# Performance work log

Measured on AMD Instinct MI355X. Metric: run time of the kernel, lower is better.

Reference implementation:

```python
import jax, jax.numpy as jnp
import numpy as np

B, N, K, D, H, FF, L, NH = 8, 50, 20, 3, 128, 2048, 3, 8
S = N * K
HD = H // NH


def setup_inputs() -> dict:
    key = jax.random.key(0)
    ks = jax.random.split(key, 16)
    visited = jax.random.uniform(ks[0], (B, S)) < 0.05
    # the single most-recent action per batch row (status flips 0 -> 1)
    action_idx = jax.random.randint(ks[1], (B,), 0, S)
    visited = visited.at[jnp.arange(B), action_idx].set(True)
    feats = jax.random.normal(ks[2], (B, S, D - 1)) * visited[:, :, None]
    state = jnp.concatenate([feats, visited[:, :, None].astype(jnp.float32)], axis=-1)
    prev_state = state.at[jnp.arange(B), action_idx, :].set(0.0)

    def w(k, shape, s=0.02):
        return jax.random.normal(k, shape, dtype=jnp.float32) * s

    return dict(
        prev_state=prev_state, state=state,
        W_pre=w(ks[3], (D, H)), b_pre=jnp.zeros(H),
        Wq=w(ks[4], (L, H, H)), bq=jnp.zeros((L, H)),
        Wk=w(ks[5], (L, H, H)), bk=jnp.zeros((L, H)),
        Wv=w(ks[6], (L, H, H)), bv=jnp.zeros((L, H)),
        Wo=w(ks[7], (L, H, H)), bo=jnp.zeros((L, H)),
        ln1_g=jnp.ones((L, H)), ln1_b=jnp.zeros((L, H)),
        Wff1=w(ks[8], (L, H, FF)), bff1=jnp.zeros((L, FF)),
        Wff2=w(ks[9], (L, FF, H)), bff2=jnp.zeros((L, H)),
        ln2_g=jnp.ones((L, H)), ln2_b=jnp.zeros((L, H)),
        W_comb=w(ks[10], (2 * H, H)), b_comb=jnp.zeros(H),
        W_dec=w(ks[11], (H, H)), b_dec=jnp.zeros(H),
        W_lin=w(ks[12], (S, S)), b_lin=jnp.zeros(S),
    )


def _layer_norm(x, g, b, eps=1e-5):
    m = jnp.mean(x, -1, keepdims=True)
    v = jnp.mean(jnp.square(x - m), -1, keepdims=True)
    return (x - m) * jax.lax.rsqrt(v + eps) * g + b


def _update_mask(state):
    # vectorized equivalent of the original Python-loop scatter mask
    status = state[:, :, -1] != 0                      # visited [B, S], S = K*N channel-major
    mask = status
    vis_kn = status.reshape(B, K, N)
    user_any = vis_kn.any(axis=1)                      # [B, N]: user visited on any channel
    mask = mask | jnp.broadcast_to(user_any[:, None, :], (B, K, N)).reshape(B, S)
    assigned = state.reshape(B, K, N, D).sum(-1) != 0  # [B, K, N]
    full = assigned.sum(-1) >= 2                       # [B, K]: channel already has 2 users
    mask = mask | jnp.broadcast_to(full[:, :, None], (B, K, N)).reshape(B, S)
    return mask


def reference(prev_state, state, W_pre, b_pre, Wq, bq, Wk, bk, Wv, bv, Wo, bo,
              ln1_g, ln1_b, Wff1, bff1, Wff2, bff2, ln2_g, ln2_b,
              W_comb, b_comb, W_dec, b_dec, W_lin, b_lin):
    mask = _update_mask(state)
    # exactly one status change per batch row (sequential RL step)
    diff = prev_state[:, :, -1] != state[:, :, -1]
    act_idx = jnp.argmax(diff, axis=1)                 # [B]

    x = state @ W_pre + b_pre                          # [B, S, H]
    scale = np.float32(1.0 / np.sqrt(HD))
    for i in range(L):  # 3 post-LN transformer encoder layers
        q = (x @ Wq[i] + bq[i]).reshape(B, S, NH, HD)
        k = (x @ Wk[i] + bk[i]).reshape(B, S, NH, HD)
        v = (x @ Wv[i] + bv[i]).reshape(B, S, NH, HD)
        att = jax.nn.softmax(jnp.einsum('bqhd,bkhd->bhqk', q, k) * scale, axis=-1)
        o = jnp.einsum('bhqk,bkhd->bqhd', att, v).reshape(B, S, H) @ Wo[i] + bo[i]
        x = _layer_norm(x + o, ln1_g[i], ln1_b[i])
        ff = jax.nn.relu(x @ Wff1[i] + bff1[i]) @ Wff2[i] + bff2[i]
        x = _layer_norm(x + ff, ln2_g[i], ln2_b[i])

    last = x[jnp.arange(B), act_idx]                   # [B, H]
    combined = jnp.concatenate([x.mean(axis=1), last], axis=-1)  # [B, 2H]
    g = combined @ W_comb + b_comb                     # [B, H]
    dec = x @ W_dec + b_dec                            # [B, S, H]
    scores = jnp.einsum('bsh,bh->bs', dec, g)          # [B, S]
    masked = scores @ W_lin + b_lin                    # Q-Learning head
    return jnp.where(mask, -jnp.inf, masked)
```

## Files before the change

kernel.cpp:

```cpp
#include <hip/hip_runtime.h>
#include <math.h>

#define Bb 8
#define Ss 1000
#define Kk 20
#define Nn 50
#define Dd 3
#define Hh 128
#define FFf 2048
#define Ll 3
#define NHh 8
#define HDd 16
#define ROWS (Bb*Ss)

#define SENTINEL -3.0e38f

typedef unsigned short ush;
typedef short short8 __attribute__((ext_vector_type(8)));
typedef short short4v __attribute__((ext_vector_type(4)));
typedef float f32x4 __attribute__((ext_vector_type(4)));

__device__ __forceinline__ ush f2b(float f) {
  unsigned x = __float_as_uint(f);
  return (ush)((x + 0x7fff + ((x >> 16) & 1)) >> 16);
}

__global__ __launch_bounds__(256) void mask_kernel(const float* __restrict__ state,
                                                   const float* __restrict__ prev_state,
                                                   int* __restrict__ mask, int* __restrict__ act_idx) {
  int b = blockIdx.x, tid = threadIdx.x;
  __shared__ unsigned char status[Ss], assigned[Ss], uany[Nn], fullk[Kk];
  __shared__ int act;
  if (tid == 0) act = 1 << 30;
  __syncthreads();
  for (int s = tid; s < Ss; s += 256) {
    const float* st = state + ((size_t)b * Ss + s) * Dd;
    float f2 = st[2];
    status[s] = (f2 != 0.f);
    assigned[s] = ((st[0] + st[1] + f2) != 0.f);
    float p2 = prev_state[((size_t)b * Ss + s) * Dd + 2];
    if (p2 != f2) atomicMin(&act, s);
  }
  __syncthreads();
  if (tid < Nn) {
    unsigned char a = 0;
    for (int k = 0; k < Kk; ++k) a |= status[k * Nn + tid];
    uany[tid] = a;
  } else if (tid >= 64 && tid < 64 + Kk) {
    int k = tid - 64, cnt = 0;
    for (int n = 0; n < Nn; ++n) cnt += assigned[k * Nn + n];
    fullk[k] = (cnt >= 2);
  }
  __syncthreads();
  for (int s = tid; s < Ss; s += 256)
    mask[b * Ss + s] = (int)(status[s] | uany[s % Nn] | fullk[s / Nn]);
  if (tid == 0) act_idx[b] = (act >= Ss) ? 0 : act;
}

__global__ __launch_bounds__(256) void pre_kernel(const float* __restrict__ state,
                                                  const float* __restrict__ W_pre,
                                                  const float* __restrict__ b_pre,
                                                  float* __restrict__ x, ush* __restrict__ xbf,
                                                  float* __restrict__ mpart) {
  int idx = blockIdx.x * 256 + threadIdx.x;
  if (idx >= ROWS * Hh) return;
  if (idx < Bb * Hh) mpart[idx] = 0.f;
  int row = idx >> 7, n = idx & 127;
  const float* st = state + (size_t)row * Dd;
  float v = b_pre[n] + st[0] * W_pre[n] + st[1] * W_pre[Hh + n] + st[2] * W_pre[2 * Hh + n];
  x[idx] = v;
  xbf[idx] = f2b(v);
}

#define TQKV 144
#define TWO  48
#define TFF1 768
#define TFF2 768
#define TWD  16
#define TBIAS 5
#define TTOT (TQKV+TWO+TFF1+TFF2+TWD+TBIAS)
__global__ __launch_bounds__(256) void transpose_prep(
    const float* __restrict__ Wq, const float* __restrict__ Wk, const float* __restrict__ Wv,
    const float* __restrict__ Wo, const float* __restrict__ Wff1, const float* __restrict__ Wff2,
    const float* __restrict__ bq, const float* __restrict__ bk, const float* __restrict__ bv,
    const float* __restrict__ W_dec,
    ush* __restrict__ wqkvT, ush* __restrict__ woT, ush* __restrict__ wff1T, ush* __restrict__ wff2T,
    float* __restrict__ bqkv, float* __restrict__ wdecT) {
  int t = blockIdx.x, tid = threadIdx.x;
  if (t >= TTOT - TBIAS) {
    int idx = (t - (TTOT - TBIAS)) * 256 + tid;
    if (idx < Ll * 384) {
      int l = idx / 384, c = idx % 384;
      bqkv[idx] = (c < 128) ? bq[l * Hh + c] : (c < 256 ? bk[l * Hh + c - 128] : bv[l * Hh + c - 256]);
    }
    return;
  }
  __shared__ float lf[32][33];
  int tr = tid >> 5, tc = tid & 31;
  const float* s; ush* d = nullptr; float* df = nullptr;
  int sp, dp;
  if (t < TQKV) {
    int l = t / 48, rem = t % 48, mat = rem / 16, tt = rem % 16;
    int ti = tt >> 2, tj = tt & 3;
    const float* m = (mat == 0) ? Wq : (mat == 1) ? Wk : Wv;
    s = m + (size_t)l * 16384 + (size_t)(ti * 32) * 128 + tj * 32; sp = 128;
    d = wqkvT + ((size_t)l * 384 + mat * 128 + tj * 32) * 128 + ti * 32; dp = 128;
  } else if (t < TQKV + TWO) {
    int r0 = t - TQKV; int l = r0 / 16, tt = r0 % 16, ti = tt >> 2, tj = tt & 3;
    s = Wo + (size_t)l * 16384 + (size_t)(ti * 32) * 128 + tj * 32; sp = 128;
    d = woT + ((size_t)l * 128 + tj * 32) * 128 + ti * 32; dp = 128;
  } else if (t < TQKV + TWO + TFF1) {
    int r0 = t - TQKV - TWO; int l = r0 / 256, tt = r0 % 256, ti = tt >> 6, tj = tt & 63;
    s = Wff1 + (size_t)l * 128 * 2048 + (size_t)(ti * 32) * 2048 + tj * 32; sp = 2048;
    d = wff1T + ((size_t)l * 2048 + tj * 32) * 128 + ti * 32; dp = 128;
  } else if (t < TQKV + TWO + TFF1 + TFF2) {
    int r0 = t - TQKV - TWO - TFF1; int l = r0 / 256, tt = r0 % 256, ti = tt >> 2, tj = tt & 3;
    s = Wff2 + (size_t)l * 2048 * 128 + (size_t)(ti * 32) * 128 + tj * 32; sp = 128;
    d = wff2T + ((size_t)l * 128 + tj * 32) * 2048 + ti * 32; dp = 2048;
  } else {
    int tt = t - TQKV - TWO - TFF1 - TFF2; int ti = tt >> 2, tj = tt & 3;
    s = W_dec + (size_t)(ti * 32) * 128 + tj * 32; sp = 128;
    df = wdecT + (size_t)(tj * 32) * 128 + ti * 32; dp = 128;
  }
#pragma unroll
  for (int p = 0; p < 4; ++p) {
    int r = tr + p * 8;
    lf[r][tc] = s[(size_t)r * sp + tc];
  }
  __syncthreads();
#pragma unroll
  for (int p = 0; p < 4; ++p) {
    int r = tr + p * 8;
    if (d) d[(size_t)r * dp + tc] = f2b(lf[tc][r]);
    else   df[(size_t)r * dp + tc] = lf[tc][r];
  }
}

#define LDP 40
template <int RELU, int QKVV>
__global__ __launch_bounds__(256) void gemm_mfma(const ush* __restrict__ A, const ush* __restrict__ Wt,
                                                 const float* __restrict__ bias, ush* __restrict__ out,
                                                 int N, int K, ush* __restrict__ vTout) {
  __shared__ ush As[2][64 * LDP];
  __shared__ ush Bs[2][64 * LDP];
  int tid = threadIdx.x;
  int lane = tid & 63, wid = tid >> 6;
  int wr = wid >> 1, wc = wid & 1;
  int m0 = blockIdx.y * 64, n0 = blockIdx.x * 64;
  int lrow = tid >> 2, lk = (tid & 3) << 3;
  int quad = lane >> 4, l16 = lane & 15, kb = quad << 3;

  const ush* Ap = A + (size_t)(m0 + lrow) * K + lk;
  const ush* Bp = Wt + (size_t)(n0 + lrow) * K + lk;

  f32x4 acc[2][2];
#pragma unroll
  for (int i = 0; i < 2; ++i)
#pragma unroll
    for (int j = 0; j < 2; ++j) acc[i][j] = (f32x4){0.f, 0.f, 0.f, 0.f};

  short8 pa = *(const short8*)Ap;
  short8 pb = *(const short8*)Bp;
  *(short8*)&As[0][lrow * LDP + lk] = pa;
  *(short8*)&Bs[0][lrow * LDP + lk] = pb;
  __syncthreads();

  int NT = K >> 5;
  for (int it = 0; it < NT; ++it) {
    int cur = it & 1;
    bool have = (it + 1 < NT);
    if (have) {
      pa = *(const short8*)(Ap + (it + 1) * 32);
      pb = *(const short8*)(Bp + (it + 1) * 32);
    }
    short8 a0 = *(short8*)&As[cur][(wr * 32 + l16) * LDP + kb];
    short8 a1 = *(short8*)&As[cur][(wr * 32 + 16 + l16) * LDP + kb];
    short8 b0 = *(short8*)&Bs[cur][(wc * 32 + l16) * LDP + kb];
    short8 b1 = *(short8*)&Bs[cur][(wc * 32 + 16 + l16) * LDP + kb];
    acc[0][0] = __builtin_amdgcn_mfma_f32_16x16x32_bf16(a0, b0, acc[0][0], 0, 0, 0);
    acc[0][1] = __builtin_amdgcn_mfma_f32_16x16x32_bf16(a0, b1, acc[0][1], 0, 0, 0);
    acc[1][0] = __builtin_amdgcn_mfma_f32_16x16x32_bf16(a1, b0, acc[1][0], 0, 0, 0);
    acc[1][1] = __builtin_amdgcn_mfma_f32_16x16x32_bf16(a1, b1, acc[1][1], 0, 0, 0);
    if (have) {
      *(short8*)&As[cur ^ 1][lrow * LDP + lk] = pa;
      *(short8*)&Bs[cur ^ 1][lrow * LDP + lk] = pb;
    }
    __syncthreads();
  }

#pragma unroll
  for (int i = 0; i < 2; ++i)
#pragma unroll
    for (int j = 0; j < 2; ++j) {
      int col = n0 + wc * 32 + j * 16 + l16;
      int rbase = m0 + wr * 32 + i * 16 + quad * 4;
      float bval = bias[col];
      if (QKVV && col >= 256) {
        int bb2 = rbase / 1000, qq = rbase - bb2 * 1000;
        short4v pk;
#pragma unroll
        for (int v = 0; v < 4; ++v) pk[v] = (short)f2b(acc[i][j][v] + bval);
        *(short4v*)&vTout[((size_t)(bb2 * 128 + (col - 256))) * 1024 + qq] = pk;
      } else {
#pragma unroll
        for (int v = 0; v < 4; ++v) {
          float o = acc[i][j][v] + bval;
          if (RELU) o = fmaxf(o, 0.f);
          out[(size_t)(rbase + v) * N + col] = f2b(o);
        }
      }
    }
}

#define F2P 72
template <int MEANOUT>
__global__ __launch_bounds__(512) void gemm_ln_kernel(const ush* __restrict__ A,
                                                      const ush* __restrict__ Wt,
                                                      const float* __restrict__ bias,
                                                      const float* __restrict__ ln_g, const float* __restrict__ ln_b,
                                                      float* __restrict__ x, ush* __restrict__ xbf,
                                                      float* __restrict__ mpart) {
  const int KK = 2048;
  __shared__ ush As[2][32 * F2P];
  __shared__ ush Bs[2][128 * F2P];
  __shared__ float red1[2][4][16], red2[2][4][16];
  __shared__ float pbias[128], pg[128], pb[128];

  int tid = threadIdx.x, lane = tid & 63, w = tid >> 6;
  int wr = w & 1, wc = w >> 1;
  int l16 = lane & 15, quad = lane >> 4, kb = quad * 8;
  int m0 = blockIdx.x * 32;
  if (tid < 128) { pbias[tid] = bias[tid]; pg[tid] = ln_g[tid]; pb[tid] = ln_b[tid]; }

  f32x4 acc[2];
  acc[0] = (f32x4){0.f, 0.f, 0.f, 0.f};
  acc[1] = (f32x4){0.f, 0.f, 0.f, 0.f};

  int arow = tid >> 3, alk = (tid & 7) << 3;
  int brow = tid >> 2, bc = (tid & 3) << 4;
  const ush* Ap = A + (size_t)(m0 + arow) * KK + alk;
  const ush* Bp = Wt + (size_t)brow * KK + bc;

  short8 ra_a, rb_a, ra_b0, ra_b1, rb_b0, rb_b1;

  if (tid < 256) ra_a = *(const short8*)Ap;
  ra_b0 = *(const short8*)Bp;
  ra_b1 = *(const short8*)(Bp + 8);
  if (tid < 256) *(short8*)&As[0][arow * F2P + alk] = ra_a;
  *(short8*)&Bs[0][brow * F2P + bc] = ra_b0;
  *(short8*)&Bs[0][brow * F2P + bc + 8] = ra_b1;
  if (tid < 256) rb_a = *(const short8*)(Ap + 64);
  rb_b0 = *(const short8*)(Bp + 64);
  rb_b1 = *(const short8*)(Bp + 64 + 8);
  __syncthreads();

  for (int k = 0; k < 16; ++k) {
    int t2 = 2 * k + 2, t3 = 2 * k + 3;
    if (t2 < 32) {
      if (tid < 256) ra_a = *(const short8*)(Ap + t2 * 64);
      ra_b0 = *(const short8*)(Bp + t2 * 64);
      ra_b1 = *(const short8*)(Bp + t2 * 64 + 8);
    }
#pragma unroll
    for (int kk = 0; kk < 2; ++kk) {
      short8 a = *(short8*)&As[0][(wr * 16 + l16) * F2P + kk * 32 + kb];
#pragma unroll
      for (int j = 0; j < 2; ++j) {
        short8 b = *(short8*)&Bs[0][(wc * 32 + j * 16 + l16) * F2P + kk * 32 + kb];
        acc[j] = __builtin_amdgcn_mfma_f32_16x16x32_bf16(a, b, acc[j], 0, 0, 0);
      }
    }
    if (tid < 256) *(short8*)&As[1][arow * F2P + alk] = rb_a;
    *(short8*)&Bs[1][brow * F2P + bc] = rb_b0;
    *(short8*)&Bs[1][brow * F2P + bc + 8] = rb_b1;
    __syncthreads();
    if (t3 < 32) {
      if (tid < 256) rb_a = *(const short8*)(Ap + t3 * 64);
      rb_b0 = *(const short8*)(Bp + t3 * 64);
      rb_b1 = *(const short8*)(Bp + t3 * 64 + 8);
    }
#pragma unroll
    for (int kk = 0; kk < 2; ++kk) {
      short8 a = *(short8*)&As[1][(wr * 16 + l16) * F2P + kk * 32 + kb];
#pragma unroll
      for (int j = 0; j < 2; ++j) {
        short8 b = *(short8*)&Bs[1][(wc * 32 + j * 16 + l16) * F2P + kk * 32 + kb];
        acc[j] = __builtin_amdgcn_mfma_f32_16x16x32_bf16(a, b, acc[j], 0, 0, 0);
      }
    }
    if (t2 < 32) {
      if (tid < 256) *(short8*)&As[0][arow * F2P + alk] = ra_a;
      *(short8*)&Bs[0][brow * F2P + bc] = ra_b0;
      *(short8*)&Bs[0][brow * F2P + bc + 8] = ra_b1;
    }
    __syncthreads();
  }

  float v[2][4], s1[4] = {0.f, 0.f, 0.f, 0.f}, s2[4] = {0.f, 0.f, 0.f, 0.f};
#pragma unroll
  for (int j = 0; j < 2; ++j) {
    int col = wc * 32 + j * 16 + l16;
#pragma unroll
    for (int r = 0; r < 4; ++r) {
      int row = m0 + wr * 16 + quad * 4 + r;
      float vv = acc[j][r] + pbias[col] + x[(size_t)row * Hh + col];
      v[j][r] = vv; s1[r] += vv; s2[r] += vv * vv;
    }
  }
#pragma unroll
  for (int m = 1; m <= 8; m <<= 1) {
#pragma unroll
    for (int r = 0; r < 4; ++r) { s1[r] += __shfl_xor(s1[r], m); s2[r] += __shfl_xor(s2[r], m); }
  }
  if (l16 == 0) {
#pragma unroll
    for (int r = 0; r < 4; ++r) {
      red1[wr][wc][quad * 4 + r] = s1[r];
      red2[wr][wc][quad * 4 + r] = s2[r];
    }
  }
  __syncthreads();
  float osum[2] = {0.f, 0.f};
#pragma unroll
  for (int r = 0; r < 4; ++r) {
    int qr = quad * 4 + r;
    float t1 = red1[wr][0][qr] + red1[wr][1][qr] + red1[wr][2][qr] + red1[wr][3][qr];
    float t2 = red2[wr][0][qr] + red2[wr][1][qr] + red2[wr][2][qr] + red2[wr][3][qr];
    float mean = t1 * (1.f / 128.f);
    float var = t2 * (1.f / 128.f) - mean * mean;
    float rstd = rsqrtf(var + 1e-5f);
    int row = m0 + wr * 16 + qr;
#pragma unroll
    for (int j = 0; j < 2; ++j) {
      int col = wc * 32 + j * 16 + l16;
      float o = (v[j][r] - mean) * rstd * pg[col] + pb[col];
      size_t gi = (size_t)row * Hh + col;
      x[gi] = o; xbf[gi] = f2b(o);
      if (MEANOUT) osum[j] += o;
    }
  }
  if (MEANOUT) {
    int gb = (m0 + wr * 16 + quad * 4) / 1000;
#pragma unroll
    for (int j = 0; j < 2; ++j)
      atomicAdd(&mpart[gb * 128 + wc * 32 + j * 16 + l16], osum[j]);
  }
}

__global__ __launch_bounds__(256) void gemm_ln16(const ush* __restrict__ A,
                                                 const ush* __restrict__ Wt,
                                                 const float* __restrict__ bias,
                                                 const float* __restrict__ ln_g, const float* __restrict__ ln_b,
                                                 float* __restrict__ x, ush* __restrict__ xbf) {
  __shared__ ush As[2][16 * F2P];
  __shared__ ush Bs[2][128 * F2P];
  __shared__ float red1[4][16], red2[4][16];
  __shared__ float pbias[128], pg[128], pb[128];

  int tid = threadIdx.x, lane = tid & 63, w = tid >> 6;
  int l16 = lane & 15, quad = lane >> 4, kb = quad * 8;
  int m0 = blockIdx.x * 16;
  if (tid < 128) { pbias[tid] = bias[tid]; pg[tid] = ln_g[tid]; pb[tid] = ln_b[tid]; }

  f32x4 acc[2];
  acc[0] = (f32x4){0.f, 0.f, 0.f, 0.f};
  acc[1] = (f32x4){0.f, 0.f, 0.f, 0.f};

  int srow = tid >> 3, slk = (tid & 7) << 3;
  const ush* Ap = A + (size_t)(m0 + srow) * 128 + slk;
  const ush* Bp = Wt + (size_t)srow * 128 + slk;

  short8 pa;
  short8 pbr[4];
  if (tid < 128) pa = *(const short8*)Ap;
#pragma unroll
  for (int rep = 0; rep < 4; ++rep)
    pbr[rep] = *(const short8*)(Bp + (size_t)rep * 32 * 128);
  if (tid < 128) *(short8*)&As[0][srow * F2P + slk] = pa;
#pragma unroll
  for (int rep = 0; rep < 4; ++rep)
    *(short8*)&Bs[0][(rep * 32 + srow) * F2P + slk] = pbr[rep];
  __syncthreads();

#pragma unroll
  for (int it = 0; it < 2; ++it) {
    if (it == 0) {
      if (tid < 128) pa = *(const short8*)(Ap + 64);
#pragma unroll
      for (int rep = 0; rep < 4; ++rep)
        pbr[rep] = *(const short8*)(Bp + (size_t)rep * 32 * 128 + 64);
    }
#pragma unroll
    for (int kk = 0; kk < 2; ++kk) {
      short8 a = *(short8*)&As[it][l16 * F2P + kk * 32 + kb];
#pragma unroll
      for (int j = 0; j < 2; ++j) {
        short8 b = *(short8*)&Bs[it][(w * 32 + j * 16 + l16) * F2P + kk * 32 + kb];
        acc[j] = __builtin_amdgcn_mfma_f32_16x16x32_bf16(a, b, acc[j], 0, 0, 0);
      }
    }
    if (it == 0) {
      if (tid < 128) *(short8*)&As[1][srow * F2P + slk] = pa;
#pragma unroll
      for (int rep = 0; rep < 4; ++rep)
        *(short8*)&Bs[1][(rep * 32 + srow) * F2P + slk] = pbr[rep];
    }
    __syncthreads();
  }

  float v[2][4], s1[4] = {0.f, 0.f, 0.f, 0.f}, s2[4] = {0.f, 0.f, 0.f, 0.f};
#pragma unroll
  for (int j = 0; j < 2; ++j) {
    int col = w * 32 + j * 16 + l16;
#pragma unroll
    for (int r = 0; r < 4; ++r) {
      int row = m0 + quad * 4 + r;
      float vv = acc[j][r] + pbias[col] + x[(size_t)row * Hh + col];
      v[j][r] = vv; s1[r] += vv; s2[r] += vv * vv;
    }
  }
#pragma unroll
  for (int m = 1; m <= 8; m <<= 1) {
#pragma unroll
    for (int r = 0; r < 4; ++r) { s1[r] += __shfl_xor(s1[r], m); s2[r] += __shfl_xor(s2[r], m); }
  }
  if (l16 == 0) {
#pragma unroll
    for (int r = 0; r < 4; ++r) {
      red1[w][quad * 4 + r] = s1[r];
      red2[w][quad * 4 + r] = s2[r];
    }
  }
  __syncthreads();
#pragma unroll
  for (int r = 0; r < 4; ++r) {
    int qr = quad * 4 + r;
    float t1 = red1[0][qr] + red1[1][qr] + red1[2][qr] + red1[3][qr];
    float t2 = red2[0][qr] + red2[1][qr] + red2[2][qr] + red2[3][qr];
    float mean = t1 * (1.f / 128.f);
    float var = t2 * (1.f / 128.f) - mean * mean;
    float rstd = rsqrtf(var + 1e-5f);
    int row = m0 + qr;
#pragma unroll
    for (int j = 0; j < 2; ++j) {
      int col = w * 32 + j * 16 + l16;
      float o = (v[j][r] - mean) * rstd * pg[col] + pb[col];
      size_t gi = (size_t)row * Hh + col;
      x[gi] = o; xbf[gi] = f2b(o);
    }
  }
}

__global__ __launch_bounds__(256) void attn_mfma(const ush* __restrict__ qkv,
                                                 const ush* __restrict__ vT,
                                                 ush* __restrict__ attn_o) {
  int blk = blockIdx.x;
  int local = blk >> 3;
  int bh = ((blk & 7) << 3) | (local >> 4);
  int qt = local & 15;
  int b = bh >> 3, h = bh & 7;
  int qbase = qt * 64;
  int tid = threadIdx.x, lane = tid & 63, w = tid >> 6;
  int l16 = lane & 15, quad = lane >> 4, kb = quad * 8;

  __shared__ ush Ks[2][64][40];
  __shared__ ush Vs[2][16][72];
  __shared__ ush Pb[4][16][72];

  if (tid < 128) {
    int row = tid >> 1, g = tid & 1;
    *(short8*)&Ks[0][row][16 + g * 8] = (short8){0, 0, 0, 0, 0, 0, 0, 0};
    *(short8*)&Ks[1][row][16 + g * 8] = (short8){0, 0, 0, 0, 0, 0, 0, 0};
  }

  int qrow = qbase + w * 16 + l16; if (qrow >= Ss) qrow = Ss - 1;
  short8 aq = *(const short8*)(qkv + (size_t)(b * Ss + qrow) * 384 + h * HDd + kb);

  int srow = tid >> 1, sg = tid & 1;
  int sd = (tid - 128) >> 3, skg = (tid - 128) & 7;
  const ush* kbase = qkv + (size_t)b * Ss * 384 + 128 + h * HDd;
  const ush* vbase = vT + (size_t)(b * 128 + h * 16) * 1024;

  if (tid < 128) {
    short8 s8 = (short8){0, 0, 0, 0, 0, 0, 0, 0};
    if (srow < Ss) s8 = *(const short8*)(kbase + (size_t)srow * 384 + sg * 8);
    *(short8*)&Ks[0][srow][sg * 8] = s8;
  } else {
    *(short8*)&Vs[0][sd][skg * 8] = *(const short8*)(vbase + (size_t)sd * 1024 + skg * 8);
  }
  __syncthreads();

  const short one_b = (short)0x3F80;
  const short8 ones = (short8){one_b, one_b, one_b, one_b, one_b, one_b, one_b, one_b};
  f32x4 acc_pv = (f32x4){0.f, 0.f, 0.f, 0.f};
  f32x4 acc_l = (f32x4){0.f, 0.f, 0.f, 0.f};
  const f32x4 zero4 = (f32x4){0.f, 0.f, 0.f, 0.f};

  for (int it = 0; it < 16; ++it) {
    int k0 = it * 64;
    int cur = it & 1, nxt = cur ^ 1;
    bool have = (it + 1 < 16);

    short8 gk, gv;
    if (have) {
      if (tid < 128) {
        gk = (short8){0, 0, 0, 0, 0, 0, 0, 0};
        int key = k0 + 64 + srow;
        if (key < Ss) gk = *(const short8*)(kbase + (size_t)key * 384 + sg * 8);
      } else {
        gv = *(const short8*)(vbase + (size_t)sd * 1024 + k0 + 64 + skg * 8);
      }
    }

    bool tail = (k0 + 64 > Ss);
#pragma unroll
    for (int kn = 0; kn < 4; ++kn) {
      short8 ak = *(short8*)&Ks[cur][kn * 16 + l16][kb];
      f32x4 s = __builtin_amdgcn_mfma_f32_16x16x32_bf16(ak, aq, zero4, 0, 0, 0);
      float p0 = __expf(s[0] * 0.25f);
      float p1 = __expf(s[1] * 0.25f);
      float p2 = __expf(s[2] * 0.25f);
      float p3 = __expf(s[3] * 0.25f);
      if (tail) {
        int keyb = k0 + kn * 16 + quad * 4;
        if (keyb + 0 >= Ss) p0 = 0.f;
        if (keyb + 1 >= Ss) p1 = 0.f;
        if (keyb + 2 >= Ss) p2 = 0.f;
        if (keyb + 3 >= Ss) p3 = 0.f;
      }
      unsigned lo, hi;
      asm("v_cvt_pk_bf16_f32 %0, %1, %2" : "=v"(lo) : "v"(p0), "v"(p1));
      asm("v_cvt_pk_bf16_f32 %0, %1, %2" : "=v"(hi) : "v"(p2), "v"(p3));
      *(uint2*)&Pb[w][l16][kn * 16 + quad * 4] = make_uint2(lo, hi);
    }

    short8 pa0 = *(short8*)&Pb[w][l16][kb];
    short8 pa1 = *(short8*)&Pb[w][l16][32 + kb];
    short8 vb0 = *(short8*)&Vs[cur][l16][kb];
    short8 vb1 = *(short8*)&Vs[cur][l16][32 + kb];
    acc_pv = __builtin_amdgcn_mfma_f32_16x16x32_bf16(pa0, vb0, acc_pv, 0, 0, 0);
    acc_pv = __builtin_amdgcn_mfma_f32_16x16x32_bf16(pa1, vb1, acc_pv, 0, 0, 0);
    acc_l = __builtin_amdgcn_mfma_f32_16x16x32_bf16(pa0, ones, acc_l, 0, 0, 0);
    acc_l = __builtin_amdgcn_mfma_f32_16x16x32_bf16(pa1, ones, acc_l, 0, 0, 0);

    if (have) {
      if (tid < 128) *(short8*)&Ks[nxt][srow][sg * 8] = gk;
      else *(short8*)&Vs[nxt][sd][skg * 8] = gv;
    }
    __syncthreads();
  }

#pragma unroll
  for (int r = 0; r < 4; ++r) {
    int q = qbase + w * 16 + quad * 4 + r;
    if (q < Ss)
      attn_o[((size_t)(b * Ss + q)) * Hh + h * HDd + l16] = f2b(acc_pv[r] / acc_l[r]);
  }
}

__global__ __launch_bounds__(128) void ghc_kernel(const float* __restrict__ x, const float* __restrict__ mpart,
                                                  const int* __restrict__ act_idx,
                                                  const float* __restrict__ W_comb, const float* __restrict__ b_comb,
                                                  const float* __restrict__ wdecT, const float* __restrict__ b_dec,
                                                  float* __restrict__ h, float* __restrict__ cb) {
  int b = blockIdx.x, n = threadIdx.x;
  __shared__ float cs[2 * Hh], gs[Hh], red[2];
  cs[n] = mpart[b * Hh + n] * (1.f / Ss);
  cs[Hh + n] = x[((size_t)b * Ss + act_idx[b]) * Hh + n];
  __syncthreads();
  float acc = b_comb[n];
  for (int j = 0; j < 2 * Hh; ++j) acc += cs[j] * W_comb[(size_t)j * Hh + n];
  gs[n] = acc;
  __syncthreads();
  float hv = 0.f;
  for (int c = 0; c < Hh; ++c) hv += wdecT[(size_t)c * Hh + n] * gs[c];
  h[b * Hh + n] = hv;
  float t = b_dec[n] * gs[n];
  for (int off = 32; off; off >>= 1) t += __shfl_down(t, off);
  if ((n & 63) == 0) red[n >> 6] = t;
  __syncthreads();
  if (n == 0) cb[b] = red[0] + red[1];
}

__global__ __launch_bounds__(256) void scores_kernel(const float* __restrict__ x, const float* __restrict__ h,
                                                     const float* __restrict__ cb, float* __restrict__ scores) {
  int wid = threadIdx.x >> 6, lane = threadIdx.x & 63;
  int row = blockIdx.x * 4 + wid;
  if (row >= ROWS) return;
  int b = row / Ss;
  const float* xr = x + (size_t)row * Hh;
  const float* hb = h + b * Hh;
  float s = xr[lane] * hb[lane] + xr[lane + 64] * hb[lane + 64];
  for (int off = 32; off; off >>= 1) s += __shfl_down(s, off);
  if (lane == 0) scores[row] = s + cb[b];
}

__global__ __launch_bounds__(256) void final_part(const float* __restrict__ scores,
                                                  const float* __restrict__ W_lin,
                                                  float* __restrict__ fpart) {
  int spc = blockIdx.x, kc = blockIdx.y;
  int tid = threadIdx.x;
  __shared__ float ss[8][125];
  for (int i = tid; i < 8 * 125; i += 256) {
    int bb = i / 125, s = i - bb * 125;
    ss[bb][s] = scores[bb * Ss + kc * 125 + s];
  }
  __syncthreads();
  if (tid < 250) {
    int sp = spc * 250 + tid;
    float acc[8];
#pragma unroll
    for (int bb = 0; bb < 8; ++bb) acc[bb] = 0.f;
    const float* wl = &W_lin[(size_t)(kc * 125) * Ss + sp];
#pragma unroll 5
    for (int s = 0; s < 125; ++s) {
      float wv = wl[(size_t)s * Ss];
#pragma unroll
      for (int bb = 0; bb < 8; ++bb) acc[bb] = fmaf(ss[bb][s], wv, acc[bb]);
    }
#pragma unroll
    for (int bb = 0; bb < 8; ++bb)
      fpart[((size_t)kc * Bb + bb) * Ss + sp] = acc[bb];
  }
}

__global__ __launch_bounds__(256) void final_combine(const float* __restrict__ fpart,
                                                     const float* __restrict__ b_lin,
                                                     const int* __restrict__ mask,
                                                     float* __restrict__ out) {
  int b = blockIdx.y;
  int sp = blockIdx.x * 256 + threadIdx.x;
  if (sp >= Ss) return;
  float acc = b_lin[sp];
#pragma unroll
  for (int kc = 0; kc < 8; ++kc) acc += fpart[((size_t)kc * Bb + b) * Ss + sp];
  out[b * Ss + sp] = mask[b * Ss + sp] ? SENTINEL : acc;
}

extern "C" void kernel_launch(void* const* d_in, const int* in_sizes, int n_in,
                              void* d_out, int out_size, void* d_ws, size_t ws_size,
                              hipStream_t stream) {
  const float* prev_state = (const float*)d_in[0];
  const float* state = (const float*)d_in[1];
  const float* W_pre = (const float*)d_in[2];
  const float* b_pre = (const float*)d_in[3];
  const float* Wq = (const float*)d_in[4];
  const float* bq = (const float*)d_in[5];
  const float* Wk = (const float*)d_in[6];
  const float* bk = (const float*)d_in[7];
  const float* Wv = (const float*)d_in[8];
  const float* bv = (const float*)d_in[9];
  const float* Wo = (const float*)d_in[10];
  const float* bo = (const float*)d_in[11];
  const float* ln1_g = (const float*)d_in[12];
  const float* ln1_b = (const float*)d_in[13];
  const float* Wff1 = (const float*)d_in[14];
  const float* bff1 = (const float*)d_in[15];
  const float* Wff2 = (const float*)d_in[16];
  const float* bff2 = (const float*)d_in[17];
  const float* ln2_g = (const float*)d_in[18];
  const float* ln2_b = (const float*)d_in[19];
  const float* W_comb = (const float*)d_in[20];
  const float* b_comb = (const float*)d_in[21];
  const float* W_dec = (const float*)d_in[22];
  const float* b_dec = (const float*)d_in[23];
  const float* W_lin = (const float*)d_in[24];
  const float* b_lin = (const float*)d_in[25];

  char* wsp = (char*)d_ws;
  auto alloc = [&](size_t bytes) { char* p = wsp; wsp += (bytes + 255) & ~(size_t)255; return p; };
  int* mask = (int*)alloc(ROWS * 4);
  int* act = (int*)alloc(Bb * 4);
  ush* wqkvT = (ush*)alloc((size_t)Ll * 384 * 128 * 2);
  ush* woT = (ush*)alloc((size_t)Ll * 128 * 128 * 2);
  ush* wff1T = (ush*)alloc((size_t)Ll * 2048 * 128 * 2);
  ush* wff2T = (ush*)alloc((size_t)Ll * 128 * 2048 * 2);
  float* bqkv = (float*)alloc((size_t)Ll * 384 * 4);
  float* wdecT = (float*)alloc((size_t)Hh * Hh * 4);
  float* x = (float*)alloc((size_t)ROWS * Hh * 4);
  ush* xbf = (ush*)alloc((size_t)ROWS * Hh * 2);
  ush* qkv_bf = (ush*)alloc((size_t)ROWS * 384 * 2);
  ush* vT = (ush*)alloc((size_t)Bb * 128 * 1024 * 2);
  ush* attn_ob = (ush*)alloc((size_t)ROWS * Hh * 2);
  float* mpart = (float*)alloc((size_t)Bb * Hh * 4);
  float* hbuf = (float*)alloc((size_t)Bb * Hh * 4);
  float* cb = (float*)alloc((size_t)Bb * 4);
  float* scores = (float*)alloc((size_t)ROWS * 4);
  float* fpart = (float*)alloc((size_t)8 * Bb * Ss * 4);
  ush* ffb = (ush*)alloc((size_t)ROWS * FFf * 2);

  transpose_prep<<<dim3(TTOT), 256, 0, stream>>>(Wq, Wk, Wv, Wo, Wff1, Wff2, bq, bk, bv, W_dec,
                                                 wqkvT, woT, wff1T, wff2T, bqkv, wdecT);
  mask_kernel<<<Bb, 256, 0, stream>>>(state, prev_state, mask, act);
  pre_kernel<<<dim3((ROWS * Hh + 255) / 256), 256, 0, stream>>>(state, W_pre, b_pre, x, xbf, mpart);

  for (int l = 0; l < Ll; ++l) {
    gemm_mfma<0, 1><<<dim3(384 / 64, ROWS / 64), 256, 0, stream>>>(
        xbf, wqkvT + (size_t)l * 384 * 128, bqkv + l * 384, qkv_bf, 384, 128, vT);
    attn_mfma<<<dim3(1024), 256, 0, stream>>>(qkv_bf, vT, attn_ob);
    gemm_ln16<<<dim3(ROWS / 16), 256, 0, stream>>>(
        attn_ob, woT + (size_t)l * 128 * 128, bo + l * Hh, ln1_g + l * Hh, ln1_b + l * Hh, x, xbf);
    gemm_mfma<1, 0><<<dim3(2048 / 64, ROWS / 64), 256, 0, stream>>>(
        xbf, wff1T + (size_t)l * 2048 * 128, bff1 + l * FFf, ffb, 2048, 128, nullptr);
    if (l == Ll - 1)
      gemm_ln_kernel<1><<<dim3(ROWS / 32), 512, 0, stream>>>(
          ffb, wff2T + (size_t)l * 128 * 2048, bff2 + l * Hh, ln2_g + l * Hh, ln2_b + l * Hh, x, xbf, mpart);
    else
      gemm_ln_kernel<0><<<dim3(ROWS / 32), 512, 0, stream>>>(
          ffb, wff2T + (size_t)l * 128 * 2048, bff2 + l * Hh, ln2_g + l * Hh, ln2_b + l * Hh, x, xbf, mpart);
  }

  ghc_kernel<<<Bb, 128, 0, stream>>>(x, mpart, act, W_comb, b_comb, wdecT, b_dec, hbuf, cb);
  scores_kernel<<<dim3(ROWS / 4), 256, 0, stream>>>(x, hbuf, cb, scores);
  final_part<<<dim3(4, 8), 256, 0, stream>>>(scores, W_lin, fpart);
  final_combine<<<dim3(4, Bb), 256, 0, stream>>>(fpart, b_lin, mask, (float*)d_out);
}
```

Measured before the change: 363.6 us.

## Fuse FF1 and FF2 GEMMs with LayerNorm, keeping the hidden activations in LDS

Replaces the separate FF1 GEMM and the FF2+LayerNorm kernel with one kernel. For each block of 32 rows it computes 64-wide chunks of the ReLU hidden layer into shared memory and feeds them straight into the FF2 accumulation, with double-buffered W1/W2 tiles. This removes the write and re-read of the 8000x2048 bf16 intermediate buffer in every layer, plus one kernel launch per layer. In exchange there are more barriers per chunk, and every block streams the full W1 and W2 weights through L2.

Result: no change. 357.0 us, median of 2 (-1.8%).

```diff
diff --git a/kernel.cpp b/kernel.cpp
--- a/kernel.cpp
+++ b/kernel.cpp
@@ -212,86 +212,139 @@
     }
 }
 
-#define F2P 72
+#define XP 136
+#define WP 72
 template <int MEANOUT>
-__global__ __launch_bounds__(512) void gemm_ln_kernel(const ush* __restrict__ A,
-                                                      const ush* __restrict__ Wt,
-                                                      const float* __restrict__ bias,
-                                                      const float* __restrict__ ln_g, const float* __restrict__ ln_b,
-                                                      float* __restrict__ x, ush* __restrict__ xbf,
-                                                      float* __restrict__ mpart) {
-  const int KK = 2048;
-  __shared__ ush As[2][32 * F2P];
-  __shared__ ush Bs[2][128 * F2P];
+__global__ __launch_bounds__(512) void ff_fused(const ush* __restrict__ xin,
+                                                const ush* __restrict__ w1T,
+                                                const ush* __restrict__ w2T,
+                                                const float* __restrict__ b1,
+                                                const float* __restrict__ bias,
+                                                const float* __restrict__ ln_g, const float* __restrict__ ln_b,
+                                                float* __restrict__ x, ush* __restrict__ xbf,
+                                                float* __restrict__ mpart) {
+  __shared__ ush xs[32][XP];
+  __shared__ ush W1L[2][64][XP];
+  __shared__ ush W2L[2][128][WP];
+  __shared__ ush hs[32][WP];
+  __shared__ float pbias[128], pg[128], pb[128];
   __shared__ float red1[2][4][16], red2[2][4][16];
-  __shared__ float pbias[128], pg[128], pb[128];
 
   int tid = threadIdx.x, lane = tid & 63, w = tid >> 6;
-  int wr = w & 1, wc = w >> 1;
+  int f = w & 3, xr = w >> 2;
   int l16 = lane & 15, quad = lane >> 4, kb = quad * 8;
   int m0 = blockIdx.x * 32;
+
+  { int row = tid >> 4, seg = (tid & 15) << 3;
+    *(short8*)&xs[row][seg] = *(const short8*)(xin + (size_t)(m0 + row) * 128 + seg); }
   if (tid < 128) { pbias[tid] = bias[tid]; pg[tid] = ln_g[tid]; pb[tid] = ln_b[tid]; }
+
+  int w1row = tid >> 3, w1seg = (tid & 7) << 3;
+  int w2row = tid >> 2, w2seg = (tid & 3) << 4;
+
+  short8 r0a, r0b, r0c, r0d, r1a, r1b, r1c, r1d;
+
+  r0a = *(const short8*)(w1T + (size_t)w1row * 128 + w1seg);
+  r0b = *(const short8*)(w1T + (size_t)w1row * 128 + w1seg + 64);
+  r0c = *(const short8*)(w2T + (size_t)w2row * 2048 + w2seg);
+  r0d = *(const short8*)(w2T + (size_t)w2row * 2048 + w2seg + 8);
+  *(short8*)&W1L[0][w1row][w1seg] = r0a;
+  *(short8*)&W1L[0][w1row][w1seg + 64] = r0b;
+  *(short8*)&W2L[0][w2row][w2seg] = r0c;
+  *(short8*)&W2L[0][w2row][w2seg + 8] = r0d;
+  r1a = *(const short8*)(w1T + (size_t)(64 + w1row) * 128 + w1seg);
+  r1b = *(const short8*)(w1T + (size_t)(64 + w1row) * 128 + w1seg + 64);
+  r1c = *(const short8*)(w2T + (size_t)w2row * 2048 + 64 + w2seg);
+  r1d = *(const short8*)(w2T + (size_t)w2row * 2048 + 64 + w2seg + 8);
+  __syncthreads();
 
   f32x4 acc[2];
   acc[0] = (f32x4){0.f, 0.f, 0.f, 0.f};
   acc[1] = (f32x4){0.f, 0.f, 0.f, 0.f};
-
-  int arow = tid >> 3, alk = (tid & 7) << 3;
-  int brow = tid >> 2, bc = (tid & 3) << 4;
-  const ush* Ap = A + (size_t)(m0 + arow) * KK + alk;
-  const ush* Bp = Wt + (size_t)brow * KK + bc;
-
-  short8 ra_a, rb_a, ra_b0, ra_b1, rb_b0, rb_b1;
-
-  if (tid < 256) ra_a = *(const short8*)Ap;
-  ra_b0 = *(const short8*)Bp;
-  ra_b1 = *(const short8*)(Bp + 8);
-  if (tid < 256) *(short8*)&As[0][arow * F2P + alk] = ra_a;
-  *(short8*)&Bs[0][brow * F2P + bc] = ra_b0;
-  *(short8*)&Bs[0][brow * F2P + bc + 8] = ra_b1;
-  if (tid < 256) rb_a = *(const short8*)(Ap + 64);
-  rb_b0 = *(const short8*)(Bp + 64);
-  rb_b1 = *(const short8*)(Bp + 64 + 8);
-  __syncthreads();
+  const f32x4 zero4 = (f32x4){0.f, 0.f, 0.f, 0.f};
 
   for (int k = 0; k < 16; ++k) {
-    int t2 = 2 * k + 2, t3 = 2 * k + 3;
-    if (t2 < 32) {
-      if (tid < 256) ra_a = *(const short8*)(Ap + t2 * 64);
-      ra_b0 = *(const short8*)(Bp + t2 * 64);
-      ra_b1 = *(const short8*)(Bp + t2 * 64 + 8);
-    }
-#pragma unroll
-    for (int kk = 0; kk < 2; ++kk) {
-      short8 a = *(short8*)&As[0][(wr * 16 + l16) * F2P + kk * 32 + kb];
+    int c0 = 2 * k, c1 = 2 * k + 1;
+    if (c0 + 2 < 32) {
+      r0a = *(const short8*)(w1T + (size_t)((c0 + 2) * 64 + w1row) * 128 + w1seg);
+      r0b = *(const short8*)(w1T + (size_t)((c0 + 2) * 64 + w1row) * 128 + w1seg + 64);
+      r0c = *(const short8*)(w2T + (size_t)w2row * 2048 + (c0 + 2) * 64 + w2seg);
+      r0d = *(const short8*)(w2T + (size_t)w2row * 2048 + (c0 + 2) * 64 + w2seg + 8);
+    }
+    {
+      f32x4 hacc = zero4;
+#pragma unroll
+      for (int ks = 0; ks < 4; ++ks) {
+        short8 a = *(short8*)&W1L[0][f * 16 + l16][ks * 32 + kb];
+        short8 b = *(short8*)&xs[xr * 16 + l16][ks * 32 + kb];
+        hacc = __builtin_amdgcn_mfma_f32_16x16x32_bf16(a, b, hacc, 0, 0, 0);
+      }
+      int ffb = c0 * 64 + f * 16 + quad * 4;
+      float4 bv1 = *(const float4*)(b1 + ffb);
+      float h0 = fmaxf(hacc[0] + bv1.x, 0.f);
+      float h1 = fmaxf(hacc[1] + bv1.y, 0.f);
+      float h2 = fmaxf(hacc[2] + bv1.z, 0.f);
+      float h3 = fmaxf(hacc[3] + bv1.w, 0.f);
+      unsigned lo, hi;
+      asm("v_cvt_pk_bf16_f32 %0, %1, %2" : "=v"(lo) : "v"(h0), "v"(h1));
+      asm("v_cvt_pk_bf16_f32 %0, %1, %2" : "=v"(hi) : "v"(h2), "v"(h3));
+      *(uint2*)&hs[xr * 16 + l16][f * 16 + quad * 4] = make_uint2(lo, hi);
+    }
+    __syncthreads();
+#pragma unroll
+    for (int ks = 0; ks < 2; ++ks) {
+      short8 a = *(short8*)&hs[xr * 16 + l16][ks * 32 + kb];
 #pragma unroll
       for (int j = 0; j < 2; ++j) {
-        short8 b = *(short8*)&Bs[0][(wc * 32 + j * 16 + l16) * F2P + kk * 32 + kb];
+        short8 b = *(short8*)&W2L[0][f * 32 + j * 16 + l16][ks * 32 + kb];
         acc[j] = __builtin_amdgcn_mfma_f32_16x16x32_bf16(a, b, acc[j], 0, 0, 0);
       }
     }
-    if (tid < 256) *(short8*)&As[1][arow * F2P + alk] = rb_a;
-    *(short8*)&Bs[1][brow * F2P + bc] = rb_b0;
-    *(short8*)&Bs[1][brow * F2P + bc + 8] = rb_b1;
+    *(short8*)&W1L[1][w1row][w1seg] = r1a;
+    *(short8*)&W1L[1][w1row][w1seg + 64] = r1b;
+    *(short8*)&W2L[1][w2row][w2seg] = r1c;
+    *(short8*)&W2L[1][w2row][w2seg + 8] = r1d;
     __syncthreads();
-    if (t3 < 32) {
-      if (tid < 256) rb_a = *(const short8*)(Ap + t3 * 64);
-      rb_b0 = *(const short8*)(Bp + t3 * 64);
-      rb_b1 = *(const short8*)(Bp + t3 * 64 + 8);
-    }
-#pragma unroll
-    for (int kk = 0; kk < 2; ++kk) {
-      short8 a = *(short8*)&As[1][(wr * 16 + l16) * F2P + kk * 32 + kb];
+    if (c1 + 2 < 32) {
+      r1a = *(const short8*)(w1T + (size_t)((c1 + 2) * 64 + w1row) * 128 + w1seg);
+      r1b = *(const short8*)(w1T + (size_t)((c1 + 2) * 64 + w1row) * 128 + w1seg + 64);
+      r1c = *(const short8*)(w2T + (size_t)w2row * 2048 + (c1 + 2) * 64 + w2seg);
+      r1d = *(const short8*)(w2T + (size_t)w2row * 2048 + (c1 + 2) * 64 + w2seg + 8);
+    }
+    {
+      f32x4 hacc = zero4;
+#pragma unroll
+      for (int ks = 0; ks < 4; ++ks) {
+        short8 a = *(short8*)&W1L[1][f * 16 + l16][ks * 32 + kb];
+        short8 b = *(short8*)&xs[xr * 16 + l16][ks * 32 + kb];
+        hacc = __builtin_amdgcn_mfma_f32_16x16x32_bf16(a, b, hacc, 0, 0, 0);
+      }
+      int ffb = c1 * 64 + f * 16 + quad * 4;
+      float4 bv1 = *(const float4*)(b1 + ffb);
+      float h0 = fmaxf(hacc[0] + bv1.x, 0.f);
+      float h1 = fmaxf(hacc[1] + bv1.y, 0.f);
+      float h2 = fmaxf(hacc[2] + bv1.z, 0.f);
+      float h3 = fmaxf(hacc[3] + bv1.w, 0.f);
+      unsigned lo, hi;
+      asm("v_cvt_pk_bf16_f32 %0, %1, %2" : "=v"(lo) : "v"(h0), "v"(h1));
+      asm("v_cvt_pk_bf16_f32 %0, %1, %2" : "=v"(hi) : "v"(h2), "v"(h3));
+      *(uint2*)&hs[xr * 16 + l16][f * 16 + quad * 4] = make_uint2(lo, hi);
+    }
+    __syncthreads();
+#pragma unroll
+    for (int ks = 0; ks < 2; ++ks) {
+      short8 a = *(short8*)&hs[xr * 16 + l16][ks * 32 + kb];
 #pragma unroll
       for (int j = 0; j < 2; ++j) {
-        short8 b = *(short8*)&Bs[1][(wc * 32 + j * 16 + l16) * F2P + kk * 32 + kb];
+        short8 b = *(short8*)&W2L[1][f * 32 + j * 16 + l16][ks * 32 + kb];
         acc[j] = __builtin_amdgcn_mfma_f32_16x16x32_bf16(a, b, acc[j], 0, 0, 0);
       }
     }
-    if (t2 < 32) {
-      if (tid < 256) *(short8*)&As[0][arow * F2P + alk] = ra_a;
-      *(short8*)&Bs[0][brow * F2P + bc] = ra_b0;
-      *(short8*)&Bs[0][brow * F2P + bc + 8] = ra_b1;
+    if (c1 + 1 < 32) {
+      *(short8*)&W1L[0][w1row][w1seg] = r0a;
+      *(short8*)&W1L[0][w1row][w1seg + 64] = r0b;
+      *(short8*)&W2L[0][w2row][w2seg] = r0c;
+      *(short8*)&W2L[0][w2row][w2seg + 8] = r0d;
     }
     __syncthreads();
   }
@@ -299,10 +352,10 @@
   float v[2][4], s1[4] = {0.f, 0.f, 0.f, 0.f}, s2[4] = {0.f, 0.f, 0.f, 0.f};
 #pragma unroll
   for (int j = 0; j < 2; ++j) {
-    int col = wc * 32 + j * 16 + l16;
+    int col = f * 32 + j * 16 + l16;
 #pragma unroll
     for (int r = 0; r < 4; ++r) {
-      int row = m0 + wr * 16 + quad * 4 + r;
+      int row = m0 + xr * 16 + quad * 4 + r;
       float vv = acc[j][r] + pbias[col] + x[(size_t)row * Hh + col];
       v[j][r] = vv; s1[r] += vv; s2[r] += vv * vv;
     }
@@ -315,8 +368,8 @@
   if (l16 == 0) {
 #pragma unroll
     for (int r = 0; r < 4; ++r) {
-      red1[wr][wc][quad * 4 + r] = s1[r];
-      red2[wr][wc][quad * 4 + r] = s2[r];
+      red1[xr][f][quad * 4 + r] = s1[r];
+      red2[xr][f][quad * 4 + r] = s2[r];
     }
   }
   __syncthreads();
@@ -324,15 +377,15 @@
 #pragma unroll
   for (int r = 0; r < 4; ++r) {
     int qr = quad * 4 + r;
-    float t1 = red1[wr][0][qr] + red1[wr][1][qr] + red1[wr][2][qr] + red1[wr][3][qr];
-    float t2 = red2[wr][0][qr] + red2[wr][1][qr] + red2[wr][2][qr] + red2[wr][3][qr];
+    float t1 = red1[xr][0][qr] + red1[xr][1][qr] + red1[xr][2][qr] + red1[xr][3][qr];
+    float t2 = red2[xr][0][qr] + red2[xr][1][qr] + red2[xr][2][qr] + red2[xr][3][qr];
     float mean = t1 * (1.f / 128.f);
     float var = t2 * (1.f / 128.f) - mean * mean;
     float rstd = rsqrtf(var + 1e-5f);
-    int row = m0 + wr * 16 + qr;
+    int row = m0 + xr * 16 + qr;
 #pragma unroll
     for (int j = 0; j < 2; ++j) {
-      int col = wc * 32 + j * 16 + l16;
+      int col = f * 32 + j * 16 + l16;
       float o = (v[j][r] - mean) * rstd * pg[col] + pb[col];
       size_t gi = (size_t)row * Hh + col;
       x[gi] = o; xbf[gi] = f2b(o);
@@ -340,13 +393,14 @@
     }
   }
   if (MEANOUT) {
-    int gb = (m0 + wr * 16 + quad * 4) / 1000;
+    int gb = (m0 + xr * 16 + quad * 4) / 1000;
 #pragma unroll
     for (int j = 0; j < 2; ++j)
-      atomicAdd(&mpart[gb * 128 + wc * 32 + j * 16 + l16], osum[j]);
-  }
-}
-
+      atomicAdd(&mpart[gb * 128 + f * 32 + j * 16 + l16], osum[j]);
+  }
+}
+
+#define F2P 72
 __global__ __launch_bounds__(256) void gemm_ln16(const ush* __restrict__ A,
                                                  const ush* __restrict__ Wt,
                                                  const float* __restrict__ bias,
@@ -687,7 +741,6 @@
   float* cb = (float*)alloc((size_t)Bb * 4);
   float* scores = (float*)alloc((size_t)ROWS * 4);
   float* fpart = (float*)alloc((size_t)8 * Bb * Ss * 4);
-  ush* ffb = (ush*)alloc((size_t)ROWS * FFf * 2);
 
   transpose_prep<<<dim3(TTOT), 256, 0, stream>>>(Wq, Wk, Wv, Wo, Wff1, Wff2, bq, bk, bv, W_dec,
                                                  wqkvT, woT, wff1T, wff2T, bqkv, wdecT);
@@ -700,14 +753,14 @@
     attn_mfma<<<dim3(1024), 256, 0, stream>>>(qkv_bf, vT, attn_ob);
     gemm_ln16<<<dim3(ROWS / 16), 256, 0, stream>>>(
         attn_ob, woT + (size_t)l * 128 * 128, bo + l * Hh, ln1_g + l * Hh, ln1_b + l * Hh, x, xbf);
-    gemm_mfma<1, 0><<<dim3(2048 / 64, ROWS / 64), 256, 0, stream>>>(
-        xbf, wff1T + (size_t)l * 2048 * 128, bff1 + l * FFf, ffb, 2048, 128, nullptr);
     if (l == Ll - 1)
-      gemm_ln_kernel<1><<<dim3(ROWS / 32), 512, 0, stream>>>(
-          ffb, wff2T + (size_t)l * 128 * 2048, bff2 + l * Hh, ln2_g + l * Hh, ln2_b + l * Hh, x, xbf, mpart);
+      ff_fused<1><<<dim3(ROWS / 32), 512, 0, stream>>>(
+          xbf, wff1T + (size_t)l * 2048 * 128, wff2T + (size_t)l * 128 * 2048,
+          bff1 + l * FFf, bff2 + l * Hh, ln2_g + l * Hh, ln2_b + l * Hh, x, xbf, mpart);
     else
-      gemm_ln_kernel<0><<<dim3(ROWS / 32), 512, 0, stream>>>(
-          ffb, wff2T + (size_t)l * 128 * 2048, bff2 + l * Hh, ln2_g + l * Hh, ln2_b + l * Hh, x, xbf, mpart);
+      ff_fused<0><<<dim3(ROWS / 32), 512, 0, stream>>>(
+          xbf, wff1T + (size_t)l * 2048 * 128, wff2T + (size_t)l * 128 * 2048,
+          bff1 + l * FFf, bff2 + l * Hh, ln2_g + l * Hh, ln2_b + l * Hh, x, xbf, mpart);
   }
 
   ghc_kernel<<<Bb, 128, 0, stream>>>(x, mpart, act, W_comb, b_comb, wdecT, b_dec, hbuf, cb);
```
